# Optimization experiments

Measured on AMD Instinct MI355X. Metric: run time of the kernel, lower is better.

## Reference

```python
import jax, jax.numpy as jnp
import numpy as np
from jax import lax

B, C, H, W = 8, 128, 128, 128


def setup_inputs() -> dict:
    key = jax.random.key(0)
    x = jax.random.normal(key, (B, C, H, W), dtype=jnp.float32)
    # fixed depthwise 3x3 binomial blur kernel, replicated per channel (OIHW, I=1)
    blur = jnp.array([[0.0625, 0.125, 0.0625],
                      [0.125,  0.25,  0.125],
                      [0.0625, 0.125, 0.0625]], dtype=jnp.float32)
    w = jnp.broadcast_to(blur, (C, 1, 3, 3)).astype(jnp.float32)
    b = jnp.zeros((C,), dtype=jnp.float32)
    return {"x": x, "w": w, "b": b}


def reference(x, w, b):
    c = x.shape[1]
    up = jnp.repeat(jnp.repeat(x, 2, axis=2), 2, axis=3)
    # ReplicationPad2d((1,1,1,1)) == edge padding of 1 on H and W
    padded = jnp.pad(up, ((0, 0), (0, 0), (1, 1), (1, 1)), mode="edge")
    # depthwise 3x3 conv, VALID (padding already applied)
    out = lax.conv_general_dilated(
        padded, w,
        window_strides=(1, 1), padding="VALID",
        dimension_numbers=("NCHW", "OIHW", "NCHW"),
        feature_group_count=c,
    )
    return out + b[None, :, None, None]
```

## Files before the change

kernel.cpp:

```cpp
#include <hip/hip_runtime.h>


constexpr int BB = 8, CC = 128, HH = 128, WW = 128;
constexpr int W2 = WW / 2;
constexpr int WO = 2 * WW;
constexpr int HO = 2 * HH;

typedef float v4f __attribute__((ext_vector_type(4)));
typedef float v2f __attribute__((ext_vector_type(2)));

__device__ __forceinline__ void hsum(float u0, float u1, float u2,
                                     float L, float X, float Y, float R,
                                     v4f& acc) {
    float u12 = u1 + u2;
    float u01 = u0 + u1;
    acc.x += u0 * L + u12 * X;
    acc.y += u01 * X + u2 * Y;
    acc.z += u0 * X + u12 * Y;
    acc.w += u01 * Y + u2 * R;
}

__global__ __launch_bounds__(256) void upblur_kernel(
    const float* __restrict__ x, const float* __restrict__ wts,
    const float* __restrict__ bias, float* __restrict__ out)
{
    const int t = blockIdx.x * blockDim.x + threadIdx.x;
    const int cp = t & (W2 - 1);
    const int r  = (t >> 6) & (HH - 1);
    const int ch = t >> 13;

    const float* wp = wts + ch * 9;
    const float w00 = wp[0], w01 = wp[1], w02 = wp[2];
    const float w10 = wp[3], w11 = wp[4], w12 = wp[5];
    const float w20 = wp[6], w21 = wp[7], w22 = wp[8];
    const float bv = bias[ch];
    const float e0 = w00,        e1 = w01,        e2 = w02;
    const float f0 = w10 + w20,  f1 = w11 + w21,  f2 = w12 + w22;
    const float g0 = w00 + w10,  g1 = w01 + w11,  g2 = w02 + w12;
    const float h0 = w20,        h1 = w21,        h2 = w22;

    const int rm = (r > 0) ? r - 1 : 0;
    const int rp = (r < HH - 1) ? r + 1 : HH - 1;
    const int c0 = 2 * cp;
    const int cl = (c0 > 0) ? c0 - 1 : 0;
    const int cr = (c0 + 2 < WW) ? c0 + 2 : WW - 1;

    #pragma unroll
    for (int b = 0; b < BB; ++b) {
        const float* xp = x + ((long long)(b * CC + ch) * HH) * WW;
        const float* row_m = xp + rm * WW;
        const float* row_0 = xp + r  * WW;
        const float* row_p = xp + rp * WW;
        const v2f vm = *reinterpret_cast<const v2f*>(row_m + c0);
        const float Lm = row_m[cl], Rm = row_m[cr];
        const v2f v0 = *reinterpret_cast<const v2f*>(row_0 + c0);
        const float L0 = row_0[cl], R0 = row_0[cr];
        const v2f vp = *reinterpret_cast<const v2f*>(row_p + c0);
        const float Lp = row_p[cl], Rp = row_p[cr];

        v4f oE = {bv, bv, bv, bv};
        hsum(e0, e1, e2, Lm, vm.x, vm.y, Rm, oE);
        hsum(f0, f1, f2, L0, v0.x, v0.y, R0, oE);

        v4f oO = {bv, bv, bv, bv};
        hsum(g0, g1, g2, L0, v0.x, v0.y, R0, oO);
        hsum(h0, h1, h2, Lp, vp.x, vp.y, Rp, oO);

        float* op = out + ((long long)(b * CC + ch) * HO + 2 * r) * WO + 4 * cp;
        __builtin_nontemporal_store(oE, reinterpret_cast<v4f*>(op));
        __builtin_nontemporal_store(oO, reinterpret_cast<v4f*>(op + WO));
    }
}

extern "C" void kernel_launch(void* const* d_in, const int* in_sizes, int n_in,
                              void* d_out, int out_size, void* d_ws, size_t ws_size,
                              hipStream_t stream) {
    const float* x    = (const float*)d_in[0];
    const float* wts  = (const float*)d_in[1];
    const float* bias = (const float*)d_in[2];
    float* out = (float*)d_out;

    const int block = 256;
    const int grid = (CC * HH * W2) / block;
    upblur_kernel<<<grid, block, 0, stream>>>(x, wts, bias, out);
}
```

Measured before the change: 342.2 us.

## Process two input rows per thread, parallelize batch, use shuffles for halo

Instead of each thread looping over all 8 batches for one input row, each thread now handles two adjacent input rows of one batch and writes four output rows. Those two rows feed four outputs, so each thread loads four rows instead of six. Left and right neighbour columns now come from wavefront shuffles rather than extra scalar global loads. The per-channel weight index is made wave-uniform via readfirstlane. The grid grows to cover batch, giving more parallelism but less work per thread, and the shuffles assume a 64-wide wavefront aligned to a full row.

```diff
diff --git a/kernel.cpp b/kernel.cpp
--- a/kernel.cpp
+++ b/kernel.cpp
@@ -3,6 +3,7 @@
 
 constexpr int BB = 8, CC = 128, HH = 128, WW = 128;
 constexpr int W2 = WW / 2;
+constexpr int H2 = HH / 2;
 constexpr int WO = 2 * WW;
 constexpr int HO = 2 * HH;
 
@@ -20,56 +21,73 @@
     acc.w += u01 * Y + u2 * R;
 }
 
+__device__ __forceinline__ void neighbors(v2f v, int lane, float& L, float& R) {
+    L = __shfl_up(v.y, 1);
+    R = __shfl_down(v.x, 1);
+    if (lane == 0)  L = v.x;
+    if (lane == 63) R = v.y;
+}
+
 __global__ __launch_bounds__(256) void upblur_kernel(
     const float* __restrict__ x, const float* __restrict__ wts,
     const float* __restrict__ bias, float* __restrict__ out)
 {
-    const int t = blockIdx.x * blockDim.x + threadIdx.x;
+    const int t  = blockIdx.x * blockDim.x + threadIdx.x;
     const int cp = t & (W2 - 1);
-    const int r  = (t >> 6) & (HH - 1);
-    const int ch = t >> 13;
+    const int tr = (t >> 6) & (H2 - 1);
+    const int ch = (t >> 12) & (CC - 1);
+    const int b  = t >> 19;
 
-    const float* wp = wts + ch * 9;
+    const int chu = __builtin_amdgcn_readfirstlane(ch);
+    const float* wp = wts + chu * 9;
     const float w00 = wp[0], w01 = wp[1], w02 = wp[2];
     const float w10 = wp[3], w11 = wp[4], w12 = wp[5];
     const float w20 = wp[6], w21 = wp[7], w22 = wp[8];
-    const float bv = bias[ch];
-    const float e0 = w00,        e1 = w01,        e2 = w02;
-    const float f0 = w10 + w20,  f1 = w11 + w21,  f2 = w12 + w22;
-    const float g0 = w00 + w10,  g1 = w01 + w11,  g2 = w02 + w12;
-    const float h0 = w20,        h1 = w21,        h2 = w22;
+    const float bv = bias[chu];
+    const float e0 = w00,       e1 = w01,       e2 = w02;
+    const float f0 = w10 + w20, f1 = w11 + w21, f2 = w12 + w22;
+    const float g0 = w00 + w10, g1 = w01 + w11, g2 = w02 + w12;
+    const float h0 = w20,       h1 = w21,       h2 = w22;
 
-    const int rm = (r > 0) ? r - 1 : 0;
-    const int rp = (r < HH - 1) ? r + 1 : HH - 1;
+    const int r0 = 2 * tr;
+    const int r1 = r0 + 1;
+    const int rm = (r0 > 0) ? r0 - 1 : 0;
+    const int rp = (r1 < HH - 1) ? r1 + 1 : HH - 1;
     const int c0 = 2 * cp;
-    const int cl = (c0 > 0) ? c0 - 1 : 0;
-    const int cr = (c0 + 2 < WW) ? c0 + 2 : WW - 1;
 
-    #pragma unroll
-    for (int b = 0; b < BB; ++b) {
-        const float* xp = x + ((long long)(b * CC + ch) * HH) * WW;
-        const float* row_m = xp + rm * WW;
-        const float* row_0 = xp + r  * WW;
-        const float* row_p = xp + rp * WW;
-        const v2f vm = *reinterpret_cast<const v2f*>(row_m + c0);
-        const float Lm = row_m[cl], Rm = row_m[cr];
-        const v2f v0 = *reinterpret_cast<const v2f*>(row_0 + c0);
-        const float L0 = row_0[cl], R0 = row_0[cr];
-        const v2f vp = *reinterpret_cast<const v2f*>(row_p + c0);
-        const float Lp = row_p[cl], Rp = row_p[cr];
+    const float* xp = x + ((long long)(b * CC + ch) * HH) * WW + c0;
+    const v2f vm = *reinterpret_cast<const v2f*>(xp + rm * WW);
+    const v2f v0 = *reinterpret_cast<const v2f*>(xp + r0 * WW);
+    const v2f v1 = *reinterpret_cast<const v2f*>(xp + r1 * WW);
+    const v2f vp = *reinterpret_cast<const v2f*>(xp + rp * WW);
 
-        v4f oE = {bv, bv, bv, bv};
-        hsum(e0, e1, e2, Lm, vm.x, vm.y, Rm, oE);
-        hsum(f0, f1, f2, L0, v0.x, v0.y, R0, oE);
+    float Lm, Rm, L0, R0, L1, R1, Lp, Rp;
+    neighbors(vm, cp, Lm, Rm);
+    neighbors(v0, cp, L0, R0);
+    neighbors(v1, cp, L1, R1);
+    neighbors(vp, cp, Lp, Rp);
 
-        v4f oO = {bv, bv, bv, bv};
-        hsum(g0, g1, g2, L0, v0.x, v0.y, R0, oO);
-        hsum(h0, h1, h2, Lp, vp.x, vp.y, Rp, oO);
+    v4f oA = {bv, bv, bv, bv};
+    hsum(e0, e1, e2, Lm, vm.x, vm.y, Rm, oA);
+    hsum(f0, f1, f2, L0, v0.x, v0.y, R0, oA);
 
-        float* op = out + ((long long)(b * CC + ch) * HO + 2 * r) * WO + 4 * cp;
-        __builtin_nontemporal_store(oE, reinterpret_cast<v4f*>(op));
-        __builtin_nontemporal_store(oO, reinterpret_cast<v4f*>(op + WO));
-    }
+    v4f oB = {bv, bv, bv, bv};
+    hsum(g0, g1, g2, L0, v0.x, v0.y, R0, oB);
+    hsum(h0, h1, h2, L1, v1.x, v1.y, R1, oB);
+
+    v4f oC = {bv, bv, bv, bv};
+    hsum(e0, e1, e2, L0, v0.x, v0.y, R0, oC);
+    hsum(f0, f1, f2, L1, v1.x, v1.y, R1, oC);
+
+    v4f oD = {bv, bv, bv, bv};
+    hsum(g0, g1, g2, L1, v1.x, v1.y, R1, oD);
+    hsum(h0, h1, h2, Lp, vp.x, vp.y, Rp, oD);
+
+    float* op = out + ((long long)(b * CC + ch) * HO + 4 * tr) * WO + 4 * cp;
+    __builtin_nontemporal_store(oA, reinterpret_cast<v4f*>(op));
+    __builtin_nontemporal_store(oB, reinterpret_cast<v4f*>(op + WO));
+    __builtin_nontemporal_store(oC, reinterpret_cast<v4f*>(op + 2 * WO));
+    __builtin_nontemporal_store(oD, reinterpret_cast<v4f*>(op + 3 * WO));
 }
 
 extern "C" void kernel_launch(void* const* d_in, const int* in_sizes, int n_in,
@@ -81,6 +99,6 @@
     float* out = (float*)d_out;
 
     const int block = 256;
-    const int grid = (CC * HH * W2) / block;
+    const int grid = (BB * CC * H2 * W2) / block;
     upblur_kernel<<<grid, block, 0, stream>>>(x, wts, bias, out);
 }
```

Result: faster. 308.7 us (-9.8%).
